# Optimization experiments

Measured on AMD Instinct MI355X. Metric: run time of the kernel, lower is better.

Reference implementation:

```python
import jax, jax.numpy as jnp
import numpy as np


def setup_inputs() -> dict:
    key = jax.random.key(0)
    x = jax.random.normal(key, (67108864,), dtype=jnp.float32)
    return {"x": x}


def reference(x):
    # Faithful to the torch module:
    #   x = x - max(x)
    #   total = sum_i (exp(x[i]) - max(x))   # max of the *shifted* x, which is 0
    #   out = exp(x) / total
    m = jnp.max(x)
    xs = x - m                       # shifted, max(xs) == 0
    ex = jnp.exp(xs)
    n = jnp.asarray(xs.shape[0], xs.dtype)
    total = jnp.sum(ex) - n * jnp.max(xs)  # the max(xs) term is 0 but kept for fidelity
    return ex / total
```

## Files before the change

kernel.cpp:

```cpp
#include <hip/hip_runtime.h>
#include <cmath>


typedef float f4v __attribute__((ext_vector_type(4)));

#define BLOCK 256
#define NBLK  8192
#define ITERS 8

__device__ __forceinline__ void combine(float& m, double& s, float m2, double s2) {
    float mn = fmaxf(m, m2);
    double e1 = (m  == mn) ? s  : s  * (double)__expf(m  - mn);
    double e2 = (m2 == mn) ? s2 : s2 * (double)__expf(m2 - mn);
    s = e1 + e2;
    m = mn;
}

__global__ __launch_bounds__(BLOCK)
void k_partials(const f4v* __restrict__ x, long n4,
                double* __restrict__ ps, float* __restrict__ pm) {
    long base = (long)blockIdx.x * (BLOCK * ITERS) + threadIdx.x;
    f4v v[ITERS];
#pragma unroll
    for (int j = 0; j < ITERS; ++j) {
        long idx = base + (long)j * BLOCK;
        if (idx < n4) v[j] = x[idx];
        else          v[j] = (f4v){-INFINITY, -INFINITY, -INFINITY, -INFINITY};
    }
    float m = -INFINITY;
#pragma unroll
    for (int j = 0; j < ITERS; ++j)
        m = fmaxf(m, fmaxf(fmaxf(v[j].x, v[j].y), fmaxf(v[j].z, v[j].w)));
    float s = 0.f;
    if (m != -INFINITY) {
#pragma unroll
        for (int j = 0; j < ITERS; ++j)
            s += __expf(v[j].x - m) + __expf(v[j].y - m) +
                 __expf(v[j].z - m) + __expf(v[j].w - m);
    }
    double sd = (double)s;
    for (int off = 32; off > 0; off >>= 1) {
        float  m2 = __shfl_down(m,  off, 64);
        double s2 = __shfl_down(sd, off, 64);
        combine(m, sd, m2, s2);
    }
    __shared__ float  sm[BLOCK / 64];
    __shared__ double ss[BLOCK / 64];
    int lane = threadIdx.x & 63;
    int wid  = threadIdx.x >> 6;
    if (lane == 0) { sm[wid] = m; ss[wid] = sd; }
    __syncthreads();
    if (threadIdx.x == 0) {
        for (int w = 1; w < BLOCK / 64; ++w) combine(m, sd, sm[w], ss[w]);
        ps[blockIdx.x] = sd;
        pm[blockIdx.x] = m;
    }
}

__global__ __launch_bounds__(1024)
void k_reduce(const double* __restrict__ ps, const float* __restrict__ pm,
              int nblk, float* __restrict__ fin) {
    float  m = -INFINITY;
    double s = 0.0;
    for (int i = threadIdx.x; i < nblk; i += 1024) combine(m, s, pm[i], ps[i]);
    for (int off = 32; off > 0; off >>= 1) {
        float  m2 = __shfl_down(m, off, 64);
        double s2 = __shfl_down(s, off, 64);
        combine(m, s, m2, s2);
    }
    __shared__ float  sm[16];
    __shared__ double ss[16];
    int lane = threadIdx.x & 63;
    int wid  = threadIdx.x >> 6;
    if (lane == 0) { sm[wid] = m; ss[wid] = s; }
    __syncthreads();
    if (threadIdx.x == 0) {
        for (int w = 1; w < 16; ++w) combine(m, s, sm[w], ss[w]);
        fin[0] = m;
        fin[1] = (float)(1.0 / s);
    }
}

__global__ __launch_bounds__(BLOCK)
void k_out(const f4v* __restrict__ x, f4v* __restrict__ o, long n4,
           const float* __restrict__ fin) {
    float m   = fin[0];
    float inv = fin[1];
    long stride = (long)gridDim.x * BLOCK;
    for (long i = (long)blockIdx.x * BLOCK + threadIdx.x; i < n4; i += stride) {
        f4v v = x[i];
        f4v r;
        r.x = __expf(v.x - m) * inv;
        r.y = __expf(v.y - m) * inv;
        r.z = __expf(v.z - m) * inv;
        r.w = __expf(v.w - m) * inv;
        __builtin_nontemporal_store(r, &o[i]);
    }
}

extern "C" void kernel_launch(void* const* d_in, const int* in_sizes, int n_in,
                              void* d_out, int out_size, void* d_ws, size_t ws_size,
                              hipStream_t stream) {
    const float* x = (const float*)d_in[0];
    float* out = (float*)d_out;
    long n  = (long)in_sizes[0];
    long n4 = n / 4;

    double* ps  = (double*)d_ws;
    float*  pm  = (float*)((char*)d_ws + NBLK * sizeof(double));
    float*  fin = (float*)((char*)d_ws + NBLK * (sizeof(double) + sizeof(float)));

    hipLaunchKernelGGL(k_partials, dim3(NBLK), dim3(BLOCK), 0, stream,
                       (const f4v*)x, n4, ps, pm);
    hipLaunchKernelGGL(k_reduce, dim3(1), dim3(1024), 0, stream, ps, pm, NBLK, fin);
    hipLaunchKernelGGL(k_out, dim3(NBLK), dim3(BLOCK), 0, stream,
                       (const f4v*)x, (f4v*)out, n4, fin);
}
```

Measured before the change: 127.1 us.

## Fuse softmax passes into cooperative kernel keeping part of input in registers

Replaces the three-kernel pipeline (partials, single-block reduce, output) with one cooperative kernel. Each thread keeps 40 float4 values in registers across a grid-wide sync, so about a third of the input is not re-read from memory in the output pass; the rest is streamed twice as before. The global max/sum combine is folded in after the grid sync, removing two kernel launches. In exchange, register pressure is high, occupancy drops to a few blocks per CU, and the remainder loop assumes the size divides evenly with no tail handling.

```diff
diff --git a/kernel.cpp b/kernel.cpp
--- a/kernel.cpp
+++ b/kernel.cpp
@@ -1,10 +1,16 @@
 #include <hip/hip_runtime.h>
+#include <hip/hip_cooperative_groups.h>
 #include <cmath>
 
+namespace cg = cooperative_groups;
+
 
 typedef float f4v __attribute__((ext_vector_type(4)));
 
 #define BLOCK 256
+#define HELD  40
+#define GMAX  512
+
 #define NBLK  8192
 #define ITERS 8
 
@@ -15,6 +21,115 @@
     s = e1 + e2;
     m = mn;
 }
+
+__global__ __launch_bounds__(BLOCK, 2)
+void k_fused(const f4v* __restrict__ x, f4v* __restrict__ o, long n4,
+             double* __restrict__ ps, float* __restrict__ pm) {
+    const int  G = gridDim.x;
+    const long T = (long)G * BLOCK;
+
+    const long hbase = (long)blockIdx.x * (BLOCK * HELD) + threadIdx.x;
+    f4v hv[HELD];
+#pragma unroll
+    for (int j = 0; j < HELD; ++j) hv[j] = x[hbase + (long)j * BLOCK];
+
+    float m = -INFINITY;
+#pragma unroll
+    for (int j = 0; j < HELD; ++j)
+        m = fmaxf(m, fmaxf(fmaxf(hv[j].x, hv[j].y), fmaxf(hv[j].z, hv[j].w)));
+    float s0 = 0.f;
+#pragma unroll
+    for (int j = 0; j < HELD; ++j)
+        s0 += __expf(hv[j].x - m) + __expf(hv[j].y - m)
+            + __expf(hv[j].z - m) + __expf(hv[j].w - m);
+    double sd = (double)s0;
+
+    const long R0   = T * HELD;
+    const long r4   = (n4 - R0) / T;
+    const int  ngrp = (int)(r4 >> 3);
+    const long rbase = R0 + (long)blockIdx.x * (BLOCK * r4) + threadIdx.x;
+    for (int g = 0; g < ngrp; ++g) {
+        f4v tv[8];
+        const long gb = rbase + (long)g * (BLOCK * 8);
+#pragma unroll
+        for (int j = 0; j < 8; ++j) tv[j] = x[gb + (long)j * BLOCK];
+        float mg = -INFINITY;
+#pragma unroll
+        for (int j = 0; j < 8; ++j)
+            mg = fmaxf(mg, fmaxf(fmaxf(tv[j].x, tv[j].y), fmaxf(tv[j].z, tv[j].w)));
+        float sg = 0.f;
+#pragma unroll
+        for (int j = 0; j < 8; ++j)
+            sg += __expf(tv[j].x - mg) + __expf(tv[j].y - mg)
+                + __expf(tv[j].z - mg) + __expf(tv[j].w - mg);
+        combine(m, sd, mg, (double)sg);
+    }
+
+    for (int off = 32; off > 0; off >>= 1) {
+        float  m2 = __shfl_down(m,  off, 64);
+        double s2 = __shfl_down(sd, off, 64);
+        combine(m, sd, m2, s2);
+    }
+    __shared__ float  sm[BLOCK / 64];
+    __shared__ double ss[BLOCK / 64];
+    const int lane = threadIdx.x & 63;
+    const int wid  = threadIdx.x >> 6;
+    if (lane == 0) { sm[wid] = m; ss[wid] = sd; }
+    __syncthreads();
+    if (threadIdx.x == 0) {
+        for (int w = 1; w < BLOCK / 64; ++w) combine(m, sd, sm[w], ss[w]);
+        ps[blockIdx.x] = sd;
+        pm[blockIdx.x] = m;
+    }
+    __threadfence();
+    cg::this_grid().sync();
+
+    float  mf = -INFINITY;
+    double sf = 0.0;
+    for (int i = threadIdx.x; i < G; i += BLOCK) combine(mf, sf, pm[i], ps[i]);
+    for (int off = 32; off > 0; off >>= 1) {
+        float  m2 = __shfl_down(mf, off, 64);
+        double s2 = __shfl_down(sf, off, 64);
+        combine(mf, sf, m2, s2);
+    }
+    if (lane == 0) { sm[wid] = mf; ss[wid] = sf; }
+    __syncthreads();
+    __shared__ float fm, fi;
+    if (threadIdx.x == 0) {
+        for (int w = 1; w < BLOCK / 64; ++w) combine(mf, sf, sm[w], ss[w]);
+        fm = mf;
+        fi = (float)(1.0 / sf);
+    }
+    __syncthreads();
+    const float M   = fm;
+    const float INV = fi;
+
+    for (int g = 0; g < ngrp; ++g) {
+        f4v tv[8];
+        const long gb = rbase + (long)g * (BLOCK * 8);
+#pragma unroll
+        for (int j = 0; j < 8; ++j) tv[j] = x[gb + (long)j * BLOCK];
+#pragma unroll
+        for (int j = 0; j < 8; ++j) {
+            f4v r;
+            r.x = __expf(tv[j].x - M) * INV;
+            r.y = __expf(tv[j].y - M) * INV;
+            r.z = __expf(tv[j].z - M) * INV;
+            r.w = __expf(tv[j].w - M) * INV;
+            __builtin_nontemporal_store(r, &o[gb + (long)j * BLOCK]);
+        }
+    }
+#pragma unroll
+    for (int j = 0; j < HELD; ++j) {
+        f4v r;
+        r.x = __expf(hv[j].x - M) * INV;
+        r.y = __expf(hv[j].y - M) * INV;
+        r.z = __expf(hv[j].z - M) * INV;
+        r.w = __expf(hv[j].w - M) * INV;
+        __builtin_nontemporal_store(r, &o[hbase + (long)j * BLOCK]);
+    }
+}
+
 
 __global__ __launch_bounds__(BLOCK)
 void k_partials(const f4v* __restrict__ x, long n4,
@@ -101,8 +216,8 @@
 extern "C" void kernel_launch(void* const* d_in, const int* in_sizes, int n_in,
                               void* d_out, int out_size, void* d_ws, size_t ws_size,
                               hipStream_t stream) {
-    const float* x = (const float*)d_in[0];
-    float* out = (float*)d_out;
+    const f4v* x = (const f4v*)d_in[0];
+    f4v* out = (f4v*)d_out;
     long n  = (long)in_sizes[0];
     long n4 = n / 4;
 
@@ -110,9 +225,45 @@
     float*  pm  = (float*)((char*)d_ws + NBLK * sizeof(double));
     float*  fin = (float*)((char*)d_ws + NBLK * (sizeof(double) + sizeof(float)));
 
-    hipLaunchKernelGGL(k_partials, dim3(NBLK), dim3(BLOCK), 0, stream,
-                       (const f4v*)x, n4, ps, pm);
-    hipLaunchKernelGGL(k_reduce, dim3(1), dim3(1024), 0, stream, ps, pm, NBLK, fin);
-    hipLaunchKernelGGL(k_out, dim3(NBLK), dim3(BLOCK), 0, stream,
-                       (const f4v*)x, (f4v*)out, n4, fin);
-}
+    static int g_grid = -1;
+    if (g_grid < 0) {
+        int nb = 0;
+        if (hipOccupancyMaxActiveBlocksPerMultiprocessor(&nb, k_fused, BLOCK, 0)
+                != hipSuccess) nb = 0;
+        int dev = 0;
+        (void)hipGetDevice(&dev);
+        hipDeviceProp_t prop{};
+        int cus = 256;
+        if (hipGetDeviceProperties(&prop, dev) == hipSuccess && prop.multiProcessorCount > 0)
+            cus = prop.multiProcessorCount;
+        long cap = (long)nb * cus;
+        if (cap >= 1) {
+            int g = GMAX;
+            while (g > 1 && g > cap) g >>= 1;
+            g_grid = g;
+        } else {
+            g_grid = 0;
+        }
+    }
+
+    bool done = false;
+    if (g_grid > 0) {
+        void* args[] = { (void*)&x, (void*)&out, (void*)&n4, (void*)&ps, (void*)&pm };
+        hipError_t err = hipLaunchCooperativeKernel((void*)k_fused, dim3(g_grid),
+                                                    dim3(BLOCK), args, 0, stream);
+        if (err == hipSuccess) {
+            done = true;
+        } else {
+            (void)hipGetLastError();
+            g_grid = 0;
+        }
+    }
+
+    if (!done) {
+        hipLaunchKernelGGL(k_partials, dim3(NBLK), dim3(BLOCK), 0, stream,
+                           x, n4, ps, pm);
+        hipLaunchKernelGGL(k_reduce, dim3(1), dim3(1024), 0, stream, ps, pm, NBLK, fin);
+        hipLaunchKernelGGL(k_out, dim3(NBLK), dim3(BLOCK), 0, stream,
+                           x, out, n4, fin);
+    }
+}
```

After: 165.5 us. 30.2% more time.
